# Kernel optimization log

Measured on AMD Instinct MI355X. Metric: run time of the kernel, lower is better.

The kernel has to match this reference:

```python
import jax, jax.numpy as jnp
import numpy as np

NUM_GROUPS = 8   # conv groups and GroupNorm groups (get_safe_groups(256,8)==8)
EPS = 1e-5


def setup_inputs() -> dict:
    key = jax.random.key(0)
    k_x, k_w, k_rw, k_ri, k_g, k_b = jax.random.split(key, 6)
    B, Cin, H, W = 8, 256, 64, 64
    E, Cout, K = 8, 256, 2
    x = jax.random.normal(k_x, (B, Cin, H, W), jnp.float32)
    # grouped conv weight: (E*Cout, Cin//groups, 3, 3)
    conv_w = jax.random.normal(k_w, (E * Cout, Cin // NUM_GROUPS, 3, 3), jnp.float32) * 0.02
    routing_weights = jax.random.uniform(k_rw, (B, K), jnp.float32)
    routing_indices = jax.random.randint(k_ri, (B, K), 0, E)
    gamma = 1.0 + 0.1 * jax.random.normal(k_g, (E, Cout), jnp.float32)
    beta = 0.1 * jax.random.normal(k_b, (E, Cout), jnp.float32)
    return {"x": x, "routing_weights": routing_weights, "routing_indices": routing_indices,
            "top_k": K, "conv_w": conv_w, "gamma": gamma, "beta": beta}


def reference(x, routing_weights, routing_indices, top_k, conv_w, gamma, beta):
    B, Cin, H, W = x.shape
    E, Cout = gamma.shape
    # fused grouped 3x3 conv, padding=1, no bias
    fused = jax.lax.conv_general_dilated(
        x, conv_w, window_strides=(1, 1), padding=((1, 1), (1, 1)),
        dimension_numbers=("NCHW", "OIHW", "NCHW"), feature_group_count=NUM_GROUPS)
    fused = fused.reshape(B, E, Cout, H, W)
    idx = routing_indices.reshape(B, top_k)
    wts = routing_weights.reshape(B, top_k)
    # gather the top_k expert outputs per sample: [B, K, Cout, H, W]
    sel = jnp.take_along_axis(fused, idx[:, :, None, None, None], axis=1)
    # per-expert GroupNorm in fp32 with gamma/beta gathered by expert id
    G = NUM_GROUPS
    xs = sel.astype(jnp.float32).reshape(B, top_k, G, Cout // G, H, W)
    mu = xs.mean(axis=(3, 4, 5), keepdims=True)
    var = xs.var(axis=(3, 4, 5), keepdims=True)
    normed = ((xs - mu) * jax.lax.rsqrt(var + EPS)).reshape(B, top_k, Cout, H, W)
    g = gamma[idx][:, :, :, None, None]   # [B, K, Cout, 1, 1]
    b = beta[idx][:, :, :, None, None]
    normed = (normed * g + b).astype(sel.dtype)
    # SiLU then weighted combine over top_k
    act = normed * jax.nn.sigmoid(normed)
    out = jnp.sum(act * wts[:, :, None, None, None], axis=1)  # [B, Cout, H, W]
    return out
```

## Files before the change

kernel.cpp:

```cpp
#include <hip/hip_runtime.h>

typedef __attribute__((ext_vector_type(8))) short bf8_t;
typedef __attribute__((ext_vector_type(4))) float f4_t;

#define KTOP  2
#define NPAIR 16
#define NG    8
#define EPSV  1e-5f
#define XSTR  40

#define OFF_XTP   0
#define OFF_WTB   1393920
#define OFF_STATS (1393920 + 294912)

__device__ __forceinline__ unsigned short f2bf(float f) {
    unsigned u = __builtin_bit_cast(unsigned, f);
    u = (u + 0x7FFFu + ((u >> 16) & 1u)) >> 16;
    return (unsigned short)u;
}

__global__ void prep(const float* __restrict__ w, const float* __restrict__ x,
                     const int* __restrict__ ridx,
                     unsigned short* __restrict__ wTb,
                     unsigned short* __restrict__ xtp,
                     float* __restrict__ stats)
{
    __shared__ float sh[32 * 288];
    const int tid = threadIdx.x;
    if (blockIdx.x < 64) {
        const int e  = blockIdx.x >> 3;
        const int cb = (blockIdx.x & 7) * 32;
        if (blockIdx.x == 0 && tid < NPAIR * NG * 2) stats[tid] = 0.f;
        const float4* src = (const float4*)(w + (size_t)(e * 256 + cb) * 288);
        for (int f = tid; f < 2304; f += 256) ((float4*)sh)[f] = src[f];
        __syncthreads();
        for (int idx = tid; idx < 9216; idx += 256) {
            int tap = idx >> 10, rem = idx & 1023, cc = rem >> 5, i = rem & 31;
            wTb[((size_t)(e * 9 + tap) * 256 + cb + cc) * 32 + i] =
                f2bf(sh[cc * 288 + i * 9 + tap]);
        }
    } else {
        float (*t)[65] = (float(*)[65])sh;
        const int idx = blockIdx.x - 64;
        const int p   = idx / 66;
        const int r   = idx - p * 66;
        const int b   = p >> 1;
        const int e   = ridx[p];
        const bool inter = (r >= 1 && r <= 64);
        if (inter) {
            const float* xb = x + (((size_t)b * 256 + e * 32) * 64 + (r - 1)) * 64;
            for (int f = tid; f < 2048; f += 256)
                t[f >> 6][f & 63] = xb[(size_t)(f >> 6) * 4096 + (f & 63)];
        }
        __syncthreads();
        unsigned short* ob = xtp + ((size_t)p * 66 + r) * (66 * XSTR);
        for (int f = tid; f < 1056; f += 256) {
            int c = f >> 4, chp = f & 15;
            ushort2 v = make_ushort2(0, 0);
            if (inter && c >= 1 && c <= 64)
                v = make_ushort2(f2bf(t[2 * chp][c - 1]), f2bf(t[2 * chp + 1][c - 1]));
            *(ushort2*)(ob + c * XSTR + chp * 2) = v;
        }
    }
}

__launch_bounds__(512, 4)
__global__ void conv_stats(const unsigned short* __restrict__ xtp,
                           const unsigned short* __restrict__ wTb,
                           const int* __restrict__ ridx,
                           float* __restrict__ stats)
{
    __shared__ short xs[4 * 66 * XSTR];

    const int tid = threadIdx.x;
    const int st  = blockIdx.x;
    const int p   = blockIdx.y;
    const int e   = ridx[p];

    {
        const unsigned short* g = xtp + ((size_t)p * 66 + st * 2) * (66 * XSTR);
        for (int f = tid; f < 1320; f += 512)
            *(bf8_t*)&xs[f * 8] = *(const bf8_t*)(g + f * 8);
    }
    __syncthreads();

    const int lane = tid & 63, l15 = lane & 15, oct = lane >> 4;
    const int wave = tid >> 6, wc = wave & 3, wsp = wave >> 2;

    const short* Ab = xs + (wsp * 66 + l15) * XSTR + oct * 8;
    const unsigned short* Bb = wTb + ((size_t)e * 9 * 256 + wc * 64 + l15) * 32 + oct * 8;

    f4_t acc[4][4];
    #pragma unroll
    for (int mi = 0; mi < 4; ++mi)
        #pragma unroll
        for (int ni = 0; ni < 4; ++ni)
            acc[mi][ni] = (f4_t){0.f, 0.f, 0.f, 0.f};

    #pragma unroll
    for (int tap = 0; tap < 9; ++tap) {
        const int dy = tap / 3, dx = tap % 3;
        bf8_t ax[4], bw[4];
        #pragma unroll
        for (int mi = 0; mi < 4; ++mi)
            ax[mi] = *(const bf8_t*)(Ab + (dy * 66 + mi * 16 + dx) * XSTR);
        #pragma unroll
        for (int ni = 0; ni < 4; ++ni)
            bw[ni] = *(const bf8_t*)(Bb + tap * 8192 + ni * 512);
        #pragma unroll
        for (int mi = 0; mi < 4; ++mi)
            #pragma unroll
            for (int ni = 0; ni < 4; ++ni)
                acc[mi][ni] = __builtin_amdgcn_mfma_f32_16x16x32_bf16(
                    ax[mi], bw[ni], acc[mi][ni], 0, 0, 0);
    }

    float s0 = 0.f, q0 = 0.f, s1 = 0.f, q1 = 0.f;
    #pragma unroll
    for (int mi = 0; mi < 4; ++mi)
        #pragma unroll
        for (int ni = 0; ni < 4; ++ni)
            #pragma unroll
            for (int r = 0; r < 4; ++r) {
                float v = acc[mi][ni][r];
                if (ni < 2) { s0 += v; q0 = fmaf(v, v, q0); }
                else        { s1 += v; q1 = fmaf(v, v, q1); }
            }
    #pragma unroll
    for (int m = 32; m >= 1; m >>= 1) {
        s0 += __shfl_xor(s0, m); q0 += __shfl_xor(q0, m);
        s1 += __shfl_xor(s1, m); q1 += __shfl_xor(q1, m);
    }
    if (lane == 0) {
        int g0 = wc * 2;
        atomicAdd(&stats[(p * 8 + g0) * 2 + 0], s0);
        atomicAdd(&stats[(p * 8 + g0) * 2 + 1], q0);
        atomicAdd(&stats[(p * 8 + g0 + 1) * 2 + 0], s1);
        atomicAdd(&stats[(p * 8 + g0 + 1) * 2 + 1], q1);
    }
}

__launch_bounds__(512, 2)
__global__ void conv_apply(const unsigned short* __restrict__ xtp,
                           const unsigned short* __restrict__ wTb,
                           const int* __restrict__ ridx,
                           const float* __restrict__ rw,
                           const float* __restrict__ gamma,
                           const float* __restrict__ beta,
                           const float* __restrict__ stats,
                           float* __restrict__ out)
{
    __shared__ short  xs[2][4 * 66 * XSTR];
    __shared__ float2 gab[2][256];

    const int tid = threadIdx.x;
    const int st  = blockIdx.x;
    const int b   = blockIdx.y;

    {
        int k = tid >> 8, c = tid & 255;
        int p = b * KTOP + k;
        int e = ridx[p];
        int g = c >> 5;
        float s  = stats[(p * 8 + g) * 2 + 0];
        float q  = stats[(p * 8 + g) * 2 + 1];
        const float cnt = 1.f / 131072.f;
        float mu  = s * cnt;
        float var = fmaf(-mu, mu, q * cnt);
        float inv = rsqrtf(var + EPSV);
        float ga  = gamma[e * 256 + c] * inv;
        float be  = fmaf(-mu, ga, beta[e * 256 + c]);
        gab[k][c] = make_float2(ga, be);
    }
    {
        const unsigned short* g0 = xtp + ((size_t)(b * KTOP + 0) * 66 + st * 2) * (66 * XSTR);
        const unsigned short* g1 = xtp + ((size_t)(b * KTOP + 1) * 66 + st * 2) * (66 * XSTR);
        for (int f = tid; f < 2640; f += 512) {
            const unsigned short* s = (f < 1320) ? (g0 + f * 8) : (g1 + (f - 1320) * 8);
            *(bf8_t*)&xs[0][f * 8] = *(const bf8_t*)s;
        }
    }
    __syncthreads();

    const int lane = tid & 63, l15 = lane & 15, oct = lane >> 4;
    const int wave = tid >> 6, wc = wave & 3, wsp = wave >> 2;

    f4_t res[4][4];
    #pragma unroll
    for (int mi = 0; mi < 4; ++mi)
        #pragma unroll
        for (int ni = 0; ni < 4; ++ni)
            res[mi][ni] = (f4_t){0.f, 0.f, 0.f, 0.f};

    #pragma unroll
    for (int k = 0; k < KTOP; ++k) {
        const int p = b * KTOP + k;
        const int e = ridx[p];
        const unsigned short* Ab = wTb + ((size_t)e * 9 * 256 + wc * 64 + l15) * 32 + oct * 8;
        const short* Bb = &xs[k][0] + (wsp * 66 + l15) * XSTR + oct * 8;

        f4_t acc[4][4];
        #pragma unroll
        for (int mi = 0; mi < 4; ++mi)
            #pragma unroll
            for (int ni = 0; ni < 4; ++ni)
                acc[mi][ni] = (f4_t){0.f, 0.f, 0.f, 0.f};

        #pragma unroll
        for (int tap = 0; tap < 9; ++tap) {
            const int dy = tap / 3, dx = tap % 3;
            bf8_t aw[4], bx[4];
            #pragma unroll
            for (int mi = 0; mi < 4; ++mi)
                aw[mi] = *(const bf8_t*)(Ab + tap * 8192 + mi * 512);
            #pragma unroll
            for (int ni = 0; ni < 4; ++ni)
                bx[ni] = *(const bf8_t*)(Bb + (dy * 66 + ni * 16 + dx) * XSTR);
            #pragma unroll
            for (int mi = 0; mi < 4; ++mi)
                #pragma unroll
                for (int ni = 0; ni < 4; ++ni)
                    acc[mi][ni] = __builtin_amdgcn_mfma_f32_16x16x32_bf16(
                        aw[mi], bx[ni], acc[mi][ni], 0, 0, 0);
        }

        const float wk = rw[p];
        #pragma unroll
        for (int mi = 0; mi < 4; ++mi) {
            float2 gb[4];
            #pragma unroll
            for (int r = 0; r < 4; ++r)
                gb[r] = gab[k][wc * 64 + mi * 16 + oct * 4 + r];
            #pragma unroll
            for (int ni = 0; ni < 4; ++ni)
                #pragma unroll
                for (int r = 0; r < 4; ++r) {
                    float n  = fmaf(acc[mi][ni][r], gb[r].x, gb[r].y);
                    float sg = __builtin_amdgcn_rcpf(1.f + __expf(-n));
                    res[mi][ni][r] = fmaf(wk * n, sg, res[mi][ni][r]);
                }
        }
    }

    const int row = st * 2 + wsp;
    #pragma unroll
    for (int mi = 0; mi < 4; ++mi)
        #pragma unroll
        for (int r = 0; r < 4; ++r) {
            float* ob = out + ((size_t)(b * 256 + wc * 64 + mi * 16 + oct * 4 + r)) * 4096
                            + row * 64 + l15;
            #pragma unroll
            for (int ni = 0; ni < 4; ++ni)
                ob[ni * 16] = res[mi][ni][r];
        }
}

extern "C" void kernel_launch(void* const* d_in, const int* in_sizes, int n_in,
                              void* d_out, int out_size, void* d_ws, size_t ws_size,
                              hipStream_t stream) {
    const float* x      = (const float*)d_in[0];
    const float* rw     = (const float*)d_in[1];
    const int*   ridx   = (const int*)  d_in[2];
    const float* conv_w = (const float*)d_in[4];
    const float* gamma  = (const float*)d_in[5];
    const float* beta   = (const float*)d_in[6];
    float* out = (float*)d_out;

    float* ws = (float*)d_ws;
    unsigned short* xtp   = (unsigned short*)(ws + OFF_XTP);
    unsigned short* wTb   = (unsigned short*)(ws + OFF_WTB);
    float*          stats = ws + OFF_STATS;

    hipLaunchKernelGGL(prep, dim3(64 + 16 * 66), dim3(256), 0, stream,
                       conv_w, x, ridx, wTb, xtp, stats);
    hipLaunchKernelGGL(conv_stats, dim3(32, 16), dim3(512), 0, stream,
                       xtp, wTb, ridx, stats);
    hipLaunchKernelGGL(conv_apply, dim3(32, 8), dim3(512), 0, stream,
                       xtp, wTb, ridx, rw, gamma, beta, stats, out);
}
```

Baseline: 150.6 us.

## Fuse prep, stats and apply into one cooperative kernel with grid syncs

Merges the three launches into a single cooperative kernel of 256 blocks that separates its phases with grid-wide syncs. The conv accumulators for both experts stay in registers between the stats phase and the apply phase, so the convolution runs once instead of twice. This removes the duplicated MFMA work and two kernel-launch gaps. In exchange it adds grid-sync overhead, and 256 blocks at two per CU leave part of the GPU idle during the prep phase while also raising register pressure.

```diff
diff --git a/kernel.cpp b/kernel.cpp
--- a/kernel.cpp
+++ b/kernel.cpp
@@ -1,11 +1,13 @@
 #include <hip/hip_runtime.h>
+#include <hip/hip_cooperative_groups.h>
+
+namespace cg = cooperative_groups;
 
 typedef __attribute__((ext_vector_type(8))) short bf8_t;
 typedef __attribute__((ext_vector_type(4))) float f4_t;
 
 #define KTOP  2
 #define NPAIR 16
-#define NG    8
 #define EPSV  1e-5f
 #define XSTR  40
 
@@ -19,227 +21,189 @@
     return (unsigned short)u;
 }
 
-__global__ void prep(const float* __restrict__ w, const float* __restrict__ x,
-                     const int* __restrict__ ridx,
-                     unsigned short* __restrict__ wTb,
-                     unsigned short* __restrict__ xtp,
-                     float* __restrict__ stats)
+union SharedU {
+    float wsh[32 * 288];
+    float xt[2][32][65];
+    struct {
+        short  xs[2][4 * 66 * XSTR];
+        float2 gab[2][256];
+    } c;
+};
+
+__launch_bounds__(512, 2)
+__global__ void fused(const float* __restrict__ x, const float* __restrict__ w,
+                      const int* __restrict__ ridx, const float* __restrict__ rw,
+                      const float* __restrict__ gamma, const float* __restrict__ beta,
+                      unsigned short* __restrict__ xtp, unsigned short* __restrict__ wTb,
+                      float* __restrict__ stats, float* __restrict__ out)
 {
-    __shared__ float sh[32 * 288];
+    __shared__ SharedU sh;
     const int tid = threadIdx.x;
-    if (blockIdx.x < 64) {
-        const int e  = blockIdx.x >> 3;
-        const int cb = (blockIdx.x & 7) * 32;
-        if (blockIdx.x == 0 && tid < NPAIR * NG * 2) stats[tid] = 0.f;
-        const float4* src = (const float4*)(w + (size_t)(e * 256 + cb) * 288);
-        for (int f = tid; f < 2304; f += 256) ((float4*)sh)[f] = src[f];
+    const int blk = blockIdx.x;
+
+    if (blk == 0 && tid < NPAIR * 8 * 2) stats[tid] = 0.f;
+    for (int u = blk; u < 592; u += 256) {
         __syncthreads();
-        for (int idx = tid; idx < 9216; idx += 256) {
-            int tap = idx >> 10, rem = idx & 1023, cc = rem >> 5, i = rem & 31;
-            wTb[((size_t)(e * 9 + tap) * 256 + cb + cc) * 32 + i] =
-                f2bf(sh[cc * 288 + i * 9 + tap]);
-        }
-    } else {
-        float (*t)[65] = (float(*)[65])sh;
-        const int idx = blockIdx.x - 64;
-        const int p   = idx / 66;
-        const int r   = idx - p * 66;
-        const int b   = p >> 1;
-        const int e   = ridx[p];
-        const bool inter = (r >= 1 && r <= 64);
-        if (inter) {
-            const float* xb = x + (((size_t)b * 256 + e * 32) * 64 + (r - 1)) * 64;
-            for (int f = tid; f < 2048; f += 256)
-                t[f >> 6][f & 63] = xb[(size_t)(f >> 6) * 4096 + (f & 63)];
-        }
-        __syncthreads();
-        unsigned short* ob = xtp + ((size_t)p * 66 + r) * (66 * XSTR);
-        for (int f = tid; f < 1056; f += 256) {
-            int c = f >> 4, chp = f & 15;
-            ushort2 v = make_ushort2(0, 0);
-            if (inter && c >= 1 && c <= 64)
-                v = make_ushort2(f2bf(t[2 * chp][c - 1]), f2bf(t[2 * chp + 1][c - 1]));
-            *(ushort2*)(ob + c * XSTR + chp * 2) = v;
-        }
-    }
-}
-
-__launch_bounds__(512, 4)
-__global__ void conv_stats(const unsigned short* __restrict__ xtp,
-                           const unsigned short* __restrict__ wTb,
-                           const int* __restrict__ ridx,
-                           float* __restrict__ stats)
-{
-    __shared__ short xs[4 * 66 * XSTR];
-
-    const int tid = threadIdx.x;
-    const int st  = blockIdx.x;
-    const int p   = blockIdx.y;
-    const int e   = ridx[p];
+        if (u < 64) {
+            const int e = u >> 3, cb = (u & 7) * 32;
+            const float4* src = (const float4*)(w + (size_t)(e * 256 + cb) * 288);
+            for (int f = tid; f < 2304; f += 512) ((float4*)sh.wsh)[f] = src[f];
+            __syncthreads();
+            for (int idx = tid; idx < 9216; idx += 512) {
+                int tap = idx >> 10, rem = idx & 1023, cc = rem >> 5, i = rem & 31;
+                wTb[((size_t)(e * 9 + tap) * 256 + cb + cc) * 32 + i] =
+                    f2bf(sh.wsh[cc * 288 + i * 9 + tap]);
+            }
+        } else {
+            const int v = u - 64;
+            const int p = v / 33, rp = v - p * 33;
+            const int h = tid >> 8, ht = tid & 255;
+            const int r = rp * 2 + h;
+            const int b = p >> 1, e = ridx[p];
+            const bool inter = (r >= 1 && r <= 64);
+            if (inter) {
+                const float* xb = x + (((size_t)b * 256 + e * 32) * 64 + (r - 1)) * 64;
+                for (int f = ht; f < 2048; f += 256)
+                    sh.xt[h][f >> 6][f & 63] = xb[(size_t)(f >> 6) * 4096 + (f & 63)];
+            }
+            __syncthreads();
+            unsigned short* ob = xtp + ((size_t)p * 66 + r) * (66 * XSTR);
+            for (int f = ht; f < 1056; f += 256) {
+                int c = f >> 4, chp = f & 15;
+                ushort2 vv = make_ushort2(0, 0);
+                if (inter && c >= 1 && c <= 64)
+                    vv = make_ushort2(f2bf(sh.xt[h][2 * chp][c - 1]),
+                                      f2bf(sh.xt[h][2 * chp + 1][c - 1]));
+                *(ushort2*)(ob + c * XSTR + chp * 2) = vv;
+            }
+        }
+    }
+    __threadfence();
+    cg::this_grid().sync();
+
+    const int st = blk & 31;
+    const int b  = blk >> 5;
 
     {
-        const unsigned short* g = xtp + ((size_t)p * 66 + st * 2) * (66 * XSTR);
-        for (int f = tid; f < 1320; f += 512)
-            *(bf8_t*)&xs[f * 8] = *(const bf8_t*)(g + f * 8);
+        const unsigned short* g0 = xtp + ((size_t)(b * KTOP + 0) * 66 + st * 2) * (66 * XSTR);
+        const unsigned short* g1 = xtp + ((size_t)(b * KTOP + 1) * 66 + st * 2) * (66 * XSTR);
+        for (int f = tid; f < 2640; f += 512) {
+            const unsigned short* s = (f < 1320) ? (g0 + f * 8) : (g1 + (f - 1320) * 8);
+            *(bf8_t*)&sh.c.xs[0][f * 8] = *(const bf8_t*)s;
+        }
     }
     __syncthreads();
 
     const int lane = tid & 63, l15 = lane & 15, oct = lane >> 4;
     const int wave = tid >> 6, wc = wave & 3, wsp = wave >> 2;
 
-    const short* Ab = xs + (wsp * 66 + l15) * XSTR + oct * 8;
-    const unsigned short* Bb = wTb + ((size_t)e * 9 * 256 + wc * 64 + l15) * 32 + oct * 8;
-
-    f4_t acc[4][4];
-    #pragma unroll
-    for (int mi = 0; mi < 4; ++mi)
-        #pragma unroll
-        for (int ni = 0; ni < 4; ++ni)
-            acc[mi][ni] = (f4_t){0.f, 0.f, 0.f, 0.f};
-
-    #pragma unroll
-    for (int tap = 0; tap < 9; ++tap) {
-        const int dy = tap / 3, dx = tap % 3;
-        bf8_t ax[4], bw[4];
+    f4_t acc[2][4][4];
+    #pragma unroll
+    for (int k = 0; k < 2; ++k)
         #pragma unroll
         for (int mi = 0; mi < 4; ++mi)
-            ax[mi] = *(const bf8_t*)(Ab + (dy * 66 + mi * 16 + dx) * XSTR);
-        #pragma unroll
-        for (int ni = 0; ni < 4; ++ni)
-            bw[ni] = *(const bf8_t*)(Bb + tap * 8192 + ni * 512);
-        #pragma unroll
-        for (int mi = 0; mi < 4; ++mi)
-            #pragma unroll
-            for (int ni = 0; ni < 4; ++ni)
-                acc[mi][ni] = __builtin_amdgcn_mfma_f32_16x16x32_bf16(
-                    ax[mi], bw[ni], acc[mi][ni], 0, 0, 0);
-    }
-
-    float s0 = 0.f, q0 = 0.f, s1 = 0.f, q1 = 0.f;
-    #pragma unroll
-    for (int mi = 0; mi < 4; ++mi)
-        #pragma unroll
-        for (int ni = 0; ni < 4; ++ni)
-            #pragma unroll
-            for (int r = 0; r < 4; ++r) {
-                float v = acc[mi][ni][r];
-                if (ni < 2) { s0 += v; q0 = fmaf(v, v, q0); }
-                else        { s1 += v; q1 = fmaf(v, v, q1); }
-            }
-    #pragma unroll
-    for (int m = 32; m >= 1; m >>= 1) {
-        s0 += __shfl_xor(s0, m); q0 += __shfl_xor(q0, m);
-        s1 += __shfl_xor(s1, m); q1 += __shfl_xor(q1, m);
-    }
+            #pragma unroll
+            for (int ni = 0; ni < 4; ++ni)
+                acc[k][mi][ni] = (f4_t){0.f, 0.f, 0.f, 0.f};
+
+    #pragma unroll
+    for (int k = 0; k < 2; ++k) {
+        const int e = ridx[b * 2 + k];
+        const unsigned short* Ab = wTb + ((size_t)e * 9 * 256 + wc * 64 + l15) * 32 + oct * 8;
+        const short* Bb = &sh.c.xs[k][0] + (wsp * 66 + l15) * XSTR + oct * 8;
+        #pragma unroll
+        for (int tap = 0; tap < 9; ++tap) {
+            const int dy = tap / 3, dx = tap % 3;
+            bf8_t aw[4], bx[4];
+            #pragma unroll
+            for (int mi = 0; mi < 4; ++mi)
+                aw[mi] = *(const bf8_t*)(Ab + tap * 8192 + mi * 512);
+            #pragma unroll
+            for (int ni = 0; ni < 4; ++ni)
+                bx[ni] = *(const bf8_t*)(Bb + (dy * 66 + ni * 16 + dx) * XSTR);
+            #pragma unroll
+            for (int mi = 0; mi < 4; ++mi)
+                #pragma unroll
+                for (int ni = 0; ni < 4; ++ni)
+                    acc[k][mi][ni] = __builtin_amdgcn_mfma_f32_16x16x32_bf16(
+                        aw[mi], bx[ni], acc[k][mi][ni], 0, 0, 0);
+        }
+    }
+
+    float sv[2][2] = {{0.f, 0.f}, {0.f, 0.f}};
+    float qv[2][2] = {{0.f, 0.f}, {0.f, 0.f}};
+    #pragma unroll
+    for (int k = 0; k < 2; ++k)
+        #pragma unroll
+        for (int mi = 0; mi < 4; ++mi) {
+            const int hf = mi >> 1;
+            #pragma unroll
+            for (int ni = 0; ni < 4; ++ni)
+                #pragma unroll
+                for (int r = 0; r < 4; ++r) {
+                    float vv = acc[k][mi][ni][r];
+                    sv[k][hf] += vv;
+                    qv[k][hf] = fmaf(vv, vv, qv[k][hf]);
+                }
+        }
+    #pragma unroll
+    for (int m = 32; m >= 1; m >>= 1)
+        #pragma unroll
+        for (int k = 0; k < 2; ++k)
+            #pragma unroll
+            for (int hf = 0; hf < 2; ++hf) {
+                sv[k][hf] += __shfl_xor(sv[k][hf], m);
+                qv[k][hf] += __shfl_xor(qv[k][hf], m);
+            }
     if (lane == 0) {
-        int g0 = wc * 2;
-        atomicAdd(&stats[(p * 8 + g0) * 2 + 0], s0);
-        atomicAdd(&stats[(p * 8 + g0) * 2 + 1], q0);
-        atomicAdd(&stats[(p * 8 + g0 + 1) * 2 + 0], s1);
-        atomicAdd(&stats[(p * 8 + g0 + 1) * 2 + 1], q1);
-    }
-}
-
-__launch_bounds__(512, 2)
-__global__ void conv_apply(const unsigned short* __restrict__ xtp,
-                           const unsigned short* __restrict__ wTb,
-                           const int* __restrict__ ridx,
-                           const float* __restrict__ rw,
-                           const float* __restrict__ gamma,
-                           const float* __restrict__ beta,
-                           const float* __restrict__ stats,
-                           float* __restrict__ out)
-{
-    __shared__ short  xs[2][4 * 66 * XSTR];
-    __shared__ float2 gab[2][256];
-
-    const int tid = threadIdx.x;
-    const int st  = blockIdx.x;
-    const int b   = blockIdx.y;
+        #pragma unroll
+        for (int k = 0; k < 2; ++k)
+            #pragma unroll
+            for (int hf = 0; hf < 2; ++hf) {
+                int p = b * 2 + k, g = wc * 2 + hf;
+                atomicAdd(&stats[(p * 8 + g) * 2 + 0], sv[k][hf]);
+                atomicAdd(&stats[(p * 8 + g) * 2 + 1], qv[k][hf]);
+            }
+    }
+    __threadfence();
+    cg::this_grid().sync();
 
     {
         int k = tid >> 8, c = tid & 255;
-        int p = b * KTOP + k;
-        int e = ridx[p];
-        int g = c >> 5;
-        float s  = stats[(p * 8 + g) * 2 + 0];
-        float q  = stats[(p * 8 + g) * 2 + 1];
+        int p = b * 2 + k, e = ridx[p], g = c >> 5;
+        float s = stats[(p * 8 + g) * 2 + 0];
+        float q = stats[(p * 8 + g) * 2 + 1];
         const float cnt = 1.f / 131072.f;
         float mu  = s * cnt;
         float var = fmaf(-mu, mu, q * cnt);
         float inv = rsqrtf(var + EPSV);
         float ga  = gamma[e * 256 + c] * inv;
         float be  = fmaf(-mu, ga, beta[e * 256 + c]);
-        gab[k][c] = make_float2(ga, be);
-    }
-    {
-        const unsigned short* g0 = xtp + ((size_t)(b * KTOP + 0) * 66 + st * 2) * (66 * XSTR);
-        const unsigned short* g1 = xtp + ((size_t)(b * KTOP + 1) * 66 + st * 2) * (66 * XSTR);
-        for (int f = tid; f < 2640; f += 512) {
-            const unsigned short* s = (f < 1320) ? (g0 + f * 8) : (g1 + (f - 1320) * 8);
-            *(bf8_t*)&xs[0][f * 8] = *(const bf8_t*)s;
-        }
+        sh.c.gab[k][c] = make_float2(ga, be);
     }
     __syncthreads();
 
-    const int lane = tid & 63, l15 = lane & 15, oct = lane >> 4;
-    const int wave = tid >> 6, wc = wave & 3, wsp = wave >> 2;
-
-    f4_t res[4][4];
-    #pragma unroll
-    for (int mi = 0; mi < 4; ++mi)
+    const float wk0 = rw[b * 2 + 0];
+    const float wk1 = rw[b * 2 + 1];
+    #pragma unroll
+    for (int mi = 0; mi < 4; ++mi) {
+        float2 g0[4], g1[4];
+        #pragma unroll
+        for (int r = 0; r < 4; ++r) {
+            g0[r] = sh.c.gab[0][wc * 64 + mi * 16 + oct * 4 + r];
+            g1[r] = sh.c.gab[1][wc * 64 + mi * 16 + oct * 4 + r];
+        }
         #pragma unroll
         for (int ni = 0; ni < 4; ++ni)
-            res[mi][ni] = (f4_t){0.f, 0.f, 0.f, 0.f};
-
-    #pragma unroll
-    for (int k = 0; k < KTOP; ++k) {
-        const int p = b * KTOP + k;
-        const int e = ridx[p];
-        const unsigned short* Ab = wTb + ((size_t)e * 9 * 256 + wc * 64 + l15) * 32 + oct * 8;
-        const short* Bb = &xs[k][0] + (wsp * 66 + l15) * XSTR + oct * 8;
-
-        f4_t acc[4][4];
-        #pragma unroll
-        for (int mi = 0; mi < 4; ++mi)
-            #pragma unroll
-            for (int ni = 0; ni < 4; ++ni)
-                acc[mi][ni] = (f4_t){0.f, 0.f, 0.f, 0.f};
-
-        #pragma unroll
-        for (int tap = 0; tap < 9; ++tap) {
-            const int dy = tap / 3, dx = tap % 3;
-            bf8_t aw[4], bx[4];
-            #pragma unroll
-            for (int mi = 0; mi < 4; ++mi)
-                aw[mi] = *(const bf8_t*)(Ab + tap * 8192 + mi * 512);
-            #pragma unroll
-            for (int ni = 0; ni < 4; ++ni)
-                bx[ni] = *(const bf8_t*)(Bb + (dy * 66 + ni * 16 + dx) * XSTR);
-            #pragma unroll
-            for (int mi = 0; mi < 4; ++mi)
-                #pragma unroll
-                for (int ni = 0; ni < 4; ++ni)
-                    acc[mi][ni] = __builtin_amdgcn_mfma_f32_16x16x32_bf16(
-                        aw[mi], bx[ni], acc[mi][ni], 0, 0, 0);
-        }
-
-        const float wk = rw[p];
-        #pragma unroll
-        for (int mi = 0; mi < 4; ++mi) {
-            float2 gb[4];
-            #pragma unroll
-            for (int r = 0; r < 4; ++r)
-                gb[r] = gab[k][wc * 64 + mi * 16 + oct * 4 + r];
-            #pragma unroll
-            for (int ni = 0; ni < 4; ++ni)
-                #pragma unroll
-                for (int r = 0; r < 4; ++r) {
-                    float n  = fmaf(acc[mi][ni][r], gb[r].x, gb[r].y);
-                    float sg = __builtin_amdgcn_rcpf(1.f + __expf(-n));
-                    res[mi][ni][r] = fmaf(wk * n, sg, res[mi][ni][r]);
-                }
-        }
+            #pragma unroll
+            for (int r = 0; r < 4; ++r) {
+                float n0  = fmaf(acc[0][mi][ni][r], g0[r].x, g0[r].y);
+                float sg0 = __builtin_amdgcn_rcpf(1.f + __expf(-n0));
+                acc[0][mi][ni][r] = wk0 * n0 * sg0;
+                float n1  = fmaf(acc[1][mi][ni][r], g1[r].x, g1[r].y);
+                float sg1 = __builtin_amdgcn_rcpf(1.f + __expf(-n1));
+                acc[0][mi][ni][r] = fmaf(wk1 * n1, sg1, acc[0][mi][ni][r]);
+            }
     }
 
     const int row = st * 2 + wsp;
@@ -251,7 +215,7 @@
                             + row * 64 + l15;
             #pragma unroll
             for (int ni = 0; ni < 4; ++ni)
-                ob[ni * 16] = res[mi][ni][r];
+                ob[ni * 16] = acc[0][mi][ni][r];
         }
 }
 
@@ -271,10 +235,9 @@
     unsigned short* wTb   = (unsigned short*)(ws + OFF_WTB);
     float*          stats = ws + OFF_STATS;
 
-    hipLaunchKernelGGL(prep, dim3(64 + 16 * 66), dim3(256), 0, stream,
-                       conv_w, x, ridx, wTb, xtp, stats);
-    hipLaunchKernelGGL(conv_stats, dim3(32, 16), dim3(512), 0, stream,
-                       xtp, wTb, ridx, stats);
-    hipLaunchKernelGGL(conv_apply, dim3(32, 8), dim3(512), 0, stream,
-                       xtp, wTb, ridx, rw, gamma, beta, stats, out);
+    void* args[] = {(void*)&x, (void*)&conv_w, (void*)&ridx, (void*)&rw,
+                    (void*)&gamma, (void*)&beta, (void*)&xtp, (void*)&wTb,
+                    (void*)&stats, (void*)&out};
+    hipLaunchCooperativeKernel((const void*)fused, dim3(256), dim3(512),
+                               args, 0, stream);
 }
```

New measurement: 290.5 us. +92.9%, slower.
